# Performance work log

Hardware: AMD Instinct MI355X
Metric: run time of the kernel (lower is better)

The kernel has to match this reference:

```python
import jax, jax.numpy as jnp
import numpy as np

C_Z = 128
C_HID = 128

def setup_inputs() -> dict:
    key = jax.random.key(0)
    ks = jax.random.split(key, 8)
    B, N = 1, 512
    z = jax.random.normal(ks[0], (B, N, N, C_Z), dtype=jnp.float32)
    mask = jnp.ones((B, N, N), dtype=jnp.float32)
    s = 0.02
    params = {
        'ln_w': jnp.ones((C_Z,), jnp.float32),
        'ln_b': jnp.zeros((C_Z,), jnp.float32),
        'W_ap': jax.random.normal(ks[1], (C_Z, C_HID), jnp.float32) * s,
        'b_ap': jnp.zeros((C_HID,), jnp.float32),
        'W_ag': jax.random.normal(ks[2], (C_Z, C_HID), jnp.float32) * s,
        'b_ag': jnp.zeros((C_HID,), jnp.float32),
        'W_bp': jax.random.normal(ks[3], (C_Z, C_HID), jnp.float32) * s,
        'b_bp': jnp.zeros((C_HID,), jnp.float32),
        'W_bg': jax.random.normal(ks[4], (C_Z, C_HID), jnp.float32) * s,
        'b_bg': jnp.zeros((C_HID,), jnp.float32),
        'W_z': jax.random.normal(ks[5], (C_HID, C_Z), jnp.float32) * s,
        'b_z': jnp.zeros((C_Z,), jnp.float32),
    }
    return {'z': z, 'mask': mask, **params}

def _layer_norm(x, w, b, eps=1e-5):
    mu = jnp.mean(x, axis=-1, keepdims=True)
    var = jnp.mean(jnp.square(x - mu), axis=-1, keepdims=True)
    return (x - mu) * jax.lax.rsqrt(var + eps) * w + b

def reference(z, mask, ln_w, ln_b, W_ap, b_ap, W_ag, b_ag, W_bp, b_bp, W_bg, b_bg, W_z, b_z):
    # z: [B, N, N, c_z], mask: [B, N, N]
    z_norm = _layer_norm(z, ln_w, ln_b)
    m = mask[..., None]  # [B, N, N, 1]
    a = (z_norm @ W_ap + b_ap) * jax.nn.sigmoid(z_norm @ W_ag + b_ag) * m
    b = (z_norm @ W_bp + b_bp) * jax.nn.sigmoid(z_norm @ W_bg + b_bg) * m
    # outgoing triangle update: per-channel batched matmul over k
    out = jnp.einsum('bikc,bkjc->bijc', a, b)
    return z + (out @ W_z + b_z)
```

## Files before the change

### kernel.cpp

```cpp
#include <hip/hip_runtime.h>
#include <hip/hip_bf16.h>
#include <cstdint>

#define NN   512
#define CZ   128
#define PTOT (NN * NN)

typedef unsigned short u16;
typedef unsigned int   u32;

using f32x4  = __attribute__((ext_vector_type(4))) float;
using bf16x8 = __attribute__((ext_vector_type(8))) __bf16;

__device__ __forceinline__ u16 f2bf(float x) {
    u32 u = __float_as_uint(x);
    u = (u + 0x7fffu + ((u >> 16) & 1u)) >> 16;
    return (u16)u;
}

__device__ __forceinline__ f32x4 mfma16(bf16x8 a, bf16x8 b, f32x4 c) {
    return __builtin_amdgcn_mfma_f32_16x16x32_bf16(a, b, c, 0, 0, 0);
}

#define GLDS16(src, dst) __builtin_amdgcn_global_load_lds(                  \
        (__attribute__((address_space(1))) void*)(src),                     \
        (__attribute__((address_space(3))) void*)(dst), 16, 0, 0)

__global__ __launch_bounds__(256) void prep_w(
    const float* __restrict__ w0, const float* __restrict__ w1,
    const float* __restrict__ w2, const float* __restrict__ w3,
    const float* __restrict__ w4, u16* __restrict__ out)
{
    const float* srcs[5] = {w0, w1, w2, w3, w4};
    const float* src = srcs[blockIdx.x];
    u16* dst = out + blockIdx.x * 16384;
    for (int idx = threadIdx.x; idx < 16384; idx += 256) {
        int n = idx >> 7, k = idx & 127;
        dst[idx] = f2bf(src[k * 128 + n]);
    }
}

__global__ __launch_bounds__(256) void ln_k(
    const float* __restrict__ z, const float* __restrict__ lnw,
    const float* __restrict__ lnb, u16* __restrict__ zn)
{
    const int t = threadIdx.x;
    const int r = t >> 2, q = t & 3;
    const long prow = (long)blockIdx.x * 64 + r;
    const float4* zp = (const float4*)(z + prow * CZ + q * 32);

    float v[32];
    float s = 0.f, s2 = 0.f;
#pragma unroll
    for (int j = 0; j < 8; ++j) {
        float4 x = zp[j];
        v[j * 4 + 0] = x.x; v[j * 4 + 1] = x.y;
        v[j * 4 + 2] = x.z; v[j * 4 + 3] = x.w;
        s  += x.x + x.y + x.z + x.w;
        s2 += x.x * x.x + x.y * x.y + x.z * x.z + x.w * x.w;
    }
    s  += __shfl_xor(s, 1);  s  += __shfl_xor(s, 2);
    s2 += __shfl_xor(s2, 1); s2 += __shfl_xor(s2, 2);
    float mu  = s * (1.f / 128.f);
    float var = s2 * (1.f / 128.f) - mu * mu;
    float rs  = rsqrtf(var + 1e-5f);

    const float4* lwp = (const float4*)(lnw + q * 32);
    const float4* lbp = (const float4*)(lnb + q * 32);
    u32 pk[16];
#pragma unroll
    for (int j = 0; j < 8; ++j) {
        float4 lw = lwp[j], lb = lbp[j];
        float a0 = (v[j * 4 + 0] - mu) * rs * lw.x + lb.x;
        float a1 = (v[j * 4 + 1] - mu) * rs * lw.y + lb.y;
        float a2 = (v[j * 4 + 2] - mu) * rs * lw.z + lb.z;
        float a3 = (v[j * 4 + 3] - mu) * rs * lw.w + lb.w;
        pk[j * 2 + 0] = (u32)f2bf(a0) | ((u32)f2bf(a1) << 16);
        pk[j * 2 + 1] = (u32)f2bf(a2) | ((u32)f2bf(a3) << 16);
    }
    uint4* dst = (uint4*)(zn + prow * CZ + q * 32);
#pragma unroll
    for (int j = 0; j < 4; ++j) {
        uint4 w4; w4.x = pk[j*4]; w4.y = pk[j*4+1]; w4.z = pk[j*4+2]; w4.w = pk[j*4+3];
        dst[j] = w4;
    }
}

__global__ __launch_bounds__(256) void proj_k(
    const u16* __restrict__ zn,   const float* __restrict__ mask,
    const u16* __restrict__ Wt,
    const float* __restrict__ b_ap, const float* __restrict__ b_ag,
    const float* __restrict__ b_bp, const float* __restrict__ b_bg,
    u16* __restrict__ Aout, u16* __restrict__ Bout)
{
    __shared__ u16  znl[64 * 128];
    __shared__ u16  tbuf[128 * 72];
    __shared__ float lmask[64];

    const int t    = threadIdx.x, l = t & 63, w = t >> 6;
    const int tile = blockIdx.x;
    const int flav = blockIdx.y;
    const int ir   = tile >> 3;
    const int k0   = (tile & 7) << 6;

    {
        const int u = l & 15;
#pragma unroll
        for (int i = 0; i < 4; ++i) {
            int row = (w << 4) + (i << 2) + (l >> 4);
            long prow = flav ? ((long)(k0 + row) * NN + ir)
                             : ((long)ir * NN + k0 + row);
            const u16* src = zn + prow * CZ + ((u ^ (row & 15)) << 3);
            GLDS16(src, &znl[((w << 4) + (i << 2)) << 7]);
        }
    }
    if (t < 64) {
        long prow = flav ? ((long)(k0 + t) * NN + ir) : ((long)ir * NN + k0 + t);
        lmask[t] = mask[prow];
    }
    __syncthreads();

    const u16* Wp = Wt + (flav * 2 + 0) * 16384;
    const u16* Wg = Wt + (flav * 2 + 1) * 16384;

    f32x4 zero4 = {0.f, 0.f, 0.f, 0.f};
    f32x4 accP[4][2], accG[4][2];
#pragma unroll
    for (int mf = 0; mf < 4; ++mf)
#pragma unroll
        for (int nf = 0; nf < 2; ++nf) { accP[mf][nf] = zero4; accG[mf][nf] = zero4; }

#pragma unroll
    for (int kk = 0; kk < 4; ++kk) {
        bf16x8 af[4];
#pragma unroll
        for (int mf = 0; mf < 4; ++mf) {
            int row = (mf << 4) + (l & 15);
            int su  = (kk * 4 + (l >> 4)) ^ (row & 15);
            af[mf] = *(const bf16x8*)&znl[(row << 7) + (su << 3)];
        }
#pragma unroll
        for (int nf = 0; nf < 2; ++nf) {
            int n  = (w << 5) + (nf << 4) + (l & 15);
            int ko = (kk << 5) + ((l >> 4) << 3);
            bf16x8 bp = *(const bf16x8*)&Wp[(n << 7) + ko];
            bf16x8 bg = *(const bf16x8*)&Wg[(n << 7) + ko];
#pragma unroll
            for (int mf = 0; mf < 4; ++mf) {
                accP[mf][nf] = mfma16(af[mf], bp, accP[mf][nf]);
                accG[mf][nf] = mfma16(af[mf], bg, accG[mf][nf]);
            }
        }
    }

    const float* bPp = flav ? b_bp : b_ap;
    const float* bGp = flav ? b_bg : b_ag;
#pragma unroll
    for (int nf = 0; nf < 2; ++nf) {
        int col = (w << 5) + (nf << 4) + (l & 15);
        float bp = bPp[col], bg = bGp[col];
#pragma unroll
        for (int mf = 0; mf < 4; ++mf) {
            int row0 = (mf << 4) + ((l >> 4) << 2);
            float av[4];
#pragma unroll
            for (int rg = 0; rg < 4; ++rg) {
                float pv = accP[mf][nf][rg] + bp;
                float gv = accG[mf][nf][rg] + bg;
                av[rg] = pv * (1.f / (1.f + __expf(-gv))) * lmask[row0 + rg];
            }
            uint2 packed;
            packed.x = (u32)f2bf(av[0]) | ((u32)f2bf(av[1]) << 16);
            packed.y = (u32)f2bf(av[2]) | ((u32)f2bf(av[3]) << 16);
            *(uint2*)&tbuf[col * 72 + row0] = packed;
        }
    }
    __syncthreads();

    u16* outp = flav ? Bout : Aout;
    const int c = t >> 1, half = t & 1;
    u16* dst = outp + (size_t)c * PTOT + (size_t)ir * NN + k0 + half * 32;
    const u16* srcb = &tbuf[c * 72 + half * 32];
#pragma unroll
    for (int e = 0; e < 4; ++e)
        *(uint4*)(dst + e * 8) = *(const uint4*)(srcb + e * 8);
}

__global__ __launch_bounds__(256) void cgemm(
    const u16* __restrict__ A, const u16* __restrict__ B, u16* __restrict__ O)
{
    __shared__ u16 ldsA[2][128 * 64];
    __shared__ u16 ldsB[2][128 * 64];

    const int t = threadIdx.x, l = t & 63, w = t >> 6;
    const int bx0 = blockIdx.x;
    const int bx  = (bx0 & 7) * 256 + (bx0 >> 3);
    const int c  = bx >> 4, ti = (bx >> 2) & 3, tj = bx & 3;
    const u16* Ab = A + (size_t)c * PTOT + (size_t)(ti * 128) * NN;
    const u16* Bb = B + (size_t)c * PTOT + (size_t)(tj * 128) * NN;

    const int lr8 = (w << 3) + (l >> 3);
    const int uu  = l & 7;

    auto stage = [&](int buf, int kt) {
#pragma unroll
        for (int ri = 0; ri < 4; ++ri) {
            int row = ri * 32 + lr8;
            const u16* sa = Ab + (size_t)row * NN + (kt << 6) + ((uu ^ (row & 7)) << 3);
            const u16* sb = Bb + (size_t)row * NN + (kt << 6) + ((uu ^ (row & 7)) << 3);
            u16* da = &ldsA[buf][(ri * 32 + (w << 3)) << 6];
            u16* db = &ldsB[buf][(ri * 32 + (w << 3)) << 6];
            GLDS16(sa, da);
            GLDS16(sb, db);
        }
    };

    const int wm = w >> 1, wn = w & 1;
    f32x4 zero4 = {0.f, 0.f, 0.f, 0.f};
    f32x4 acc[4][4];
#pragma unroll
    for (int mf = 0; mf < 4; ++mf)
#pragma unroll
        for (int nf = 0; nf < 4; ++nf) acc[mf][nf] = zero4;

    stage(0, 0);
    __syncthreads();
    int cur = 0;
    for (int kt = 0; kt < 8; ++kt) {
        if (kt < 7) stage(cur ^ 1, kt + 1);
        const u16* lA = ldsA[cur];
        const u16* lB = ldsB[cur];
#pragma unroll
        for (int kk = 0; kk < 2; ++kk) {
            bf16x8 af[4], bfr[4];
#pragma unroll
            for (int mf = 0; mf < 4; ++mf) {
                int row = (wm << 6) + (mf << 4) + (l & 15);
                int su  = ((kk << 2) + (l >> 4)) ^ (row & 7);
                af[mf] = *(const bf16x8*)&lA[(row << 6) + (su << 3)];
            }
#pragma unroll
            for (int nf = 0; nf < 4; ++nf) {
                int row = (wn << 6) + (nf << 4) + (l & 15);
                int su  = ((kk << 2) + (l >> 4)) ^ (row & 7);
                bfr[nf] = *(const bf16x8*)&lB[(row << 6) + (su << 3)];
            }
#pragma unroll
            for (int mf = 0; mf < 4; ++mf)
#pragma unroll
                for (int nf = 0; nf < 4; ++nf)
                    acc[mf][nf] = mfma16(af[mf], bfr[nf], acc[mf][nf]);
        }
        if (kt < 7) __syncthreads();
        cur ^= 1;
    }

    u16* Ob = O + (size_t)c * PTOT;
    const int i0 = ti * 128 + (wm << 6);
    const int j0 = tj * 128 + (wn << 6);
#pragma unroll
    for (int mf = 0; mf < 4; ++mf)
#pragma unroll
        for (int nf = 0; nf < 4; ++nf) {
            int jc = j0 + (nf << 4) + (l & 15);
#pragma unroll
            for (int rg = 0; rg < 4; ++rg) {
                int irow = i0 + (mf << 4) + ((l >> 4) << 2) + rg;
                Ob[(size_t)irow * NN + jc] = f2bf(acc[mf][nf][rg]);
            }
        }
}

__global__ __launch_bounds__(256) void finalk(
    const u16* __restrict__ O, const u16* __restrict__ Wzt,
    const float* __restrict__ z, const float* __restrict__ bz,
    float* __restrict__ out)
{
    __shared__ u16 Ot[128 * 128];

    const int t = threadIdx.x, l = t & 63, w = t >> 6;
    const int p0 = blockIdx.x << 7;

    {
        const int po = t & 15;
        const int uc = t >> 4;
        uint4 q[8];
#pragma unroll
        for (int cc = 0; cc < 8; ++cc)
            q[cc] = *(const uint4*)(O + (size_t)(uc * 8 + cc) * PTOT + p0 + po * 8);
#pragma unroll
        for (int e = 0; e < 8; ++e) {
            const int sh = (e & 1) * 16;
            const int wd = e >> 1;
            u32 h[8];
#pragma unroll
            for (int cc = 0; cc < 8; ++cc)
                h[cc] = (((const u32*)&q[cc])[wd] >> sh) & 0xffffu;
            uint4 o;
            o.x = h[0] | (h[1] << 16);
            o.y = h[2] | (h[3] << 16);
            o.z = h[4] | (h[5] << 16);
            o.w = h[6] | (h[7] << 16);
            int p  = po * 8 + e;
            int su = uc ^ (p & 15) ^ ((p >> 4) & 7);
            *(uint4*)&Ot[(p << 7) + (su << 3)] = o;
        }
    }
    __syncthreads();

    f32x4 zero4 = {0.f, 0.f, 0.f, 0.f};
    f32x4 acc[8][2];
#pragma unroll
    for (int m = 0; m < 8; ++m)
#pragma unroll
        for (int np = 0; np < 2; ++np) acc[m][np] = zero4;

#pragma unroll
    for (int kk = 0; kk < 4; ++kk) {
        bf16x8 af[8];
#pragma unroll
        for (int m = 0; m < 8; ++m) {
            int co = (m << 4) + (l & 15);
            af[m] = *(const bf16x8*)&Wzt[(co << 7) + (kk << 5) + ((l >> 4) << 3)];
        }
#pragma unroll
        for (int np = 0; np < 2; ++np) {
            int p  = (w << 5) + (np << 4) + (l & 15);
            int su = ((kk << 2) + (l >> 4)) ^ (p & 15) ^ ((p >> 4) & 7);
            bf16x8 bfr = *(const bf16x8*)&Ot[(p << 7) + (su << 3)];
#pragma unroll
            for (int m = 0; m < 8; ++m)
                acc[m][np] = mfma16(af[m], bfr, acc[m][np]);
        }
    }

#pragma unroll
    for (int m = 0; m < 8; ++m) {
        const int co4 = (m << 4) + ((l >> 4) << 2);
        const float4 bv = *(const float4*)&bz[co4];
#pragma unroll
        for (int np = 0; np < 2; ++np) {
            int p = p0 + (w << 5) + (np << 4) + (l & 15);
            size_t idx = (size_t)p * CZ + co4;
            float4 zv = *(const float4*)&z[idx];
            float4 ov;
            ov.x = zv.x + acc[m][np][0] + bv.x;
            ov.y = zv.y + acc[m][np][1] + bv.y;
            ov.z = zv.z + acc[m][np][2] + bv.z;
            ov.w = zv.w + acc[m][np][3] + bv.w;
            *(float4*)&out[idx] = ov;
        }
    }
}

extern "C" void kernel_launch(void* const* d_in, const int* in_sizes, int n_in,
                              void* d_out, int out_size, void* d_ws, size_t ws_size,
                              hipStream_t stream)
{
    const float* z    = (const float*)d_in[0];
    const float* mask = (const float*)d_in[1];
    const float* lnw  = (const float*)d_in[2];
    const float* lnb  = (const float*)d_in[3];
    const float* Wap  = (const float*)d_in[4];
    const float* bap  = (const float*)d_in[5];
    const float* Wag  = (const float*)d_in[6];
    const float* bag  = (const float*)d_in[7];
    const float* Wbp  = (const float*)d_in[8];
    const float* bbp  = (const float*)d_in[9];
    const float* Wbg  = (const float*)d_in[10];
    const float* bbg  = (const float*)d_in[11];
    const float* Wz   = (const float*)d_in[12];
    const float* bz   = (const float*)d_in[13];
    float* out = (float*)d_out;

    u16* A_t  = (u16*)d_ws;
    u16* B_tt = A_t  + (size_t)CZ * PTOT;
    u16* O_t  = B_tt + (size_t)CZ * PTOT;
    u16* Wt   = O_t  + (size_t)CZ * PTOT;
    u16* Wzt  = Wt + 4 * 16384;
    u16* zn   = O_t;

    prep_w<<<5, 256, 0, stream>>>(Wap, Wag, Wbp, Wbg, Wz, Wt);
    ln_k<<<4096, 256, 0, stream>>>(z, lnw, lnb, zn);
    proj_k<<<dim3(4096, 2), 256, 0, stream>>>(zn, mask, Wt,
                                              bap, bag, bbp, bbg, A_t, B_tt);
    cgemm<<<2048, 256, 0, stream>>>(A_t, B_tt, O_t);
    finalk<<<2048, 256, 0, stream>>>(O_t, Wzt, z, bz, out);
}
```

Before: 536.8 us.

## Make proj_k process four tiles per block with double-buffered LDS staging

The projection kernel now launches 2048 blocks instead of 8192. Each block loops over four consecutive tiles, remapped across the two A/B flavours. While the current tile runs its MFMAs and gating epilogue, the next tile's normalized-z rows and mask are loaded asynchronously into a second LDS buffer. This aims to hide global-load latency and amortize block launch cost. The price is doubled znl LDS, which may lower occupancy, plus less inter-block parallelism.

```diff
diff --git a/kernel.cpp b/kernel.cpp
--- a/kernel.cpp
+++ b/kernel.cpp
@@ -93,17 +93,18 @@
     const float* __restrict__ b_bp, const float* __restrict__ b_bg,
     u16* __restrict__ Aout, u16* __restrict__ Bout)
 {
-    __shared__ u16  znl[64 * 128];
+    __shared__ u16  znl[2][64 * 128];
     __shared__ u16  tbuf[128 * 72];
-    __shared__ float lmask[64];
-
-    const int t    = threadIdx.x, l = t & 63, w = t >> 6;
-    const int tile = blockIdx.x;
-    const int flav = blockIdx.y;
-    const int ir   = tile >> 3;
-    const int k0   = (tile & 7) << 6;
-
-    {
+    __shared__ float lmask[2][64];
+
+    const int t = threadIdx.x, l = t & 63, w = t >> 6;
+
+    const int bx  = (blockIdx.x & 7) * 256 + (blockIdx.x >> 3);
+    const int uid0 = bx * 4;
+
+    auto stageU = [&](int buf, int uid) {
+        const int flav = uid >> 12, tile = uid & 4095;
+        const int ir = tile >> 3, k0 = (tile & 7) << 6;
         const int u = l & 15;
 #pragma unroll
         for (int i = 0; i < 4; ++i) {
@@ -111,79 +112,98 @@
             long prow = flav ? ((long)(k0 + row) * NN + ir)
                              : ((long)ir * NN + k0 + row);
             const u16* src = zn + prow * CZ + ((u ^ (row & 15)) << 3);
-            GLDS16(src, &znl[((w << 4) + (i << 2)) << 7]);
-        }
-    }
-    if (t < 64) {
-        long prow = flav ? ((long)(k0 + t) * NN + ir) : ((long)ir * NN + k0 + t);
-        lmask[t] = mask[prow];
-    }
-    __syncthreads();
-
-    const u16* Wp = Wt + (flav * 2 + 0) * 16384;
-    const u16* Wg = Wt + (flav * 2 + 1) * 16384;
-
-    f32x4 zero4 = {0.f, 0.f, 0.f, 0.f};
-    f32x4 accP[4][2], accG[4][2];
-#pragma unroll
-    for (int mf = 0; mf < 4; ++mf)
-#pragma unroll
-        for (int nf = 0; nf < 2; ++nf) { accP[mf][nf] = zero4; accG[mf][nf] = zero4; }
-
-#pragma unroll
-    for (int kk = 0; kk < 4; ++kk) {
-        bf16x8 af[4];
-#pragma unroll
-        for (int mf = 0; mf < 4; ++mf) {
-            int row = (mf << 4) + (l & 15);
-            int su  = (kk * 4 + (l >> 4)) ^ (row & 15);
-            af[mf] = *(const bf16x8*)&znl[(row << 7) + (su << 3)];
-        }
+            GLDS16(src, &znl[buf][((w << 4) + (i << 2)) << 7]);
+        }
+    };
+    auto maskU = [&](int buf, int uid) {
+        if (t < 64) {
+            const int flav = uid >> 12, tile = uid & 4095;
+            const int ir = tile >> 3, k0 = (tile & 7) << 6;
+            long prow = flav ? ((long)(k0 + t) * NN + ir) : ((long)ir * NN + k0 + t);
+            lmask[buf][t] = mask[prow];
+        }
+    };
+
+    stageU(0, uid0);
+    maskU(0, uid0);
+
+    int cur = 0;
+    for (int i = 0; i < 4; ++i) {
+        const int uid  = uid0 + i;
+        const int flav = uid >> 12, tile = uid & 4095;
+        const int ir   = tile >> 3, k0 = (tile & 7) << 6;
+
+        __syncthreads();
+
+        if (i < 3) { stageU(cur ^ 1, uid + 1); maskU(cur ^ 1, uid + 1); }
+
+        const u16* Wp = Wt + (flav * 2 + 0) * 16384;
+        const u16* Wg = Wt + (flav * 2 + 1) * 16384;
+
+        f32x4 zero4 = {0.f, 0.f, 0.f, 0.f};
+        f32x4 accP[4][2], accG[4][2];
+#pragma unroll
+        for (int mf = 0; mf < 4; ++mf)
+#pragma unroll
+            for (int nf = 0; nf < 2; ++nf) { accP[mf][nf] = zero4; accG[mf][nf] = zero4; }
+
+#pragma unroll
+        for (int kk = 0; kk < 4; ++kk) {
+            bf16x8 af[4];
+#pragma unroll
+            for (int mf = 0; mf < 4; ++mf) {
+                int row = (mf << 4) + (l & 15);
+                int su  = (kk * 4 + (l >> 4)) ^ (row & 15);
+                af[mf] = *(const bf16x8*)&znl[cur][(row << 7) + (su << 3)];
+            }
+#pragma unroll
+            for (int nf = 0; nf < 2; ++nf) {
+                int n  = (w << 5) + (nf << 4) + (l & 15);
+                int ko = (kk << 5) + ((l >> 4) << 3);
+                bf16x8 bp = *(const bf16x8*)&Wp[(n << 7) + ko];
+                bf16x8 bg = *(const bf16x8*)&Wg[(n << 7) + ko];
+#pragma unroll
+                for (int mf = 0; mf < 4; ++mf) {
+                    accP[mf][nf] = mfma16(af[mf], bp, accP[mf][nf]);
+                    accG[mf][nf] = mfma16(af[mf], bg, accG[mf][nf]);
+                }
+            }
+        }
+
+        const float* bPp = flav ? b_bp : b_ap;
+        const float* bGp = flav ? b_bg : b_ag;
 #pragma unroll
         for (int nf = 0; nf < 2; ++nf) {
-            int n  = (w << 5) + (nf << 4) + (l & 15);
-            int ko = (kk << 5) + ((l >> 4) << 3);
-            bf16x8 bp = *(const bf16x8*)&Wp[(n << 7) + ko];
-            bf16x8 bg = *(const bf16x8*)&Wg[(n << 7) + ko];
+            int col = (w << 5) + (nf << 4) + (l & 15);
+            float bp = bPp[col], bg = bGp[col];
 #pragma unroll
             for (int mf = 0; mf < 4; ++mf) {
-                accP[mf][nf] = mfma16(af[mf], bp, accP[mf][nf]);
-                accG[mf][nf] = mfma16(af[mf], bg, accG[mf][nf]);
-            }
-        }
-    }
-
-    const float* bPp = flav ? b_bp : b_ap;
-    const float* bGp = flav ? b_bg : b_ag;
-#pragma unroll
-    for (int nf = 0; nf < 2; ++nf) {
-        int col = (w << 5) + (nf << 4) + (l & 15);
-        float bp = bPp[col], bg = bGp[col];
-#pragma unroll
-        for (int mf = 0; mf < 4; ++mf) {
-            int row0 = (mf << 4) + ((l >> 4) << 2);
-            float av[4];
-#pragma unroll
-            for (int rg = 0; rg < 4; ++rg) {
-                float pv = accP[mf][nf][rg] + bp;
-                float gv = accG[mf][nf][rg] + bg;
-                av[rg] = pv * (1.f / (1.f + __expf(-gv))) * lmask[row0 + rg];
-            }
-            uint2 packed;
-            packed.x = (u32)f2bf(av[0]) | ((u32)f2bf(av[1]) << 16);
-            packed.y = (u32)f2bf(av[2]) | ((u32)f2bf(av[3]) << 16);
-            *(uint2*)&tbuf[col * 72 + row0] = packed;
-        }
-    }
-    __syncthreads();
-
-    u16* outp = flav ? Bout : Aout;
-    const int c = t >> 1, half = t & 1;
-    u16* dst = outp + (size_t)c * PTOT + (size_t)ir * NN + k0 + half * 32;
-    const u16* srcb = &tbuf[c * 72 + half * 32];
-#pragma unroll
-    for (int e = 0; e < 4; ++e)
-        *(uint4*)(dst + e * 8) = *(const uint4*)(srcb + e * 8);
+                int row0 = (mf << 4) + ((l >> 4) << 2);
+                float av[4];
+#pragma unroll
+                for (int rg = 0; rg < 4; ++rg) {
+                    float pv = accP[mf][nf][rg] + bp;
+                    float gv = accG[mf][nf][rg] + bg;
+                    av[rg] = pv * (1.f / (1.f + __expf(-gv))) * lmask[cur][row0 + rg];
+                }
+                uint2 packed;
+                packed.x = (u32)f2bf(av[0]) | ((u32)f2bf(av[1]) << 16);
+                packed.y = (u32)f2bf(av[2]) | ((u32)f2bf(av[3]) << 16);
+                *(uint2*)&tbuf[col * 72 + row0] = packed;
+            }
+        }
+        __syncthreads();
+
+        u16* outp = flav ? Bout : Aout;
+        const int c = t >> 1, half = t & 1;
+        u16* dst = outp + (size_t)c * PTOT + (size_t)ir * NN + k0 + half * 32;
+        const u16* srcb = &tbuf[c * 72 + half * 32];
+#pragma unroll
+        for (int e = 0; e < 4; ++e)
+            *(uint4*)(dst + e * 8) = *(const uint4*)(srcb + e * 8);
+
+        cur ^= 1;
+    }
 }
 
 __global__ __launch_bounds__(256) void cgemm(
@@ -382,8 +402,8 @@
 
     prep_w<<<5, 256, 0, stream>>>(Wap, Wag, Wbp, Wbg, Wz, Wt);
     ln_k<<<4096, 256, 0, stream>>>(z, lnw, lnb, zn);
-    proj_k<<<dim3(4096, 2), 256, 0, stream>>>(zn, mask, Wt,
-                                              bap, bag, bbp, bbg, A_t, B_tt);
+    proj_k<<<2048, 256, 0, stream>>>(zn, mask, Wt,
+                                     bap, bag, bbp, bbg, A_t, B_tt);
     cgemm<<<2048, 256, 0, stream>>>(A_t, B_tt, O_t);
     finalk<<<2048, 256, 0, stream>>>(O_t, Wzt, z, bz, out);
 }
```

Result: faster. 506.0 us (-5.7%).
